# Performance work log

Measured on AMD Instinct MI355X. Metric: run time of the kernel, lower is better.

Reference implementation:

```python
import jax, jax.numpy as jnp
import numpy as np

H = 4096          # hidden_size
I = 14336         # intermediate_size
G = 128           # quantization group size along the input dim


def dequant(q, s, g=G):
    """Dequantize group-scaled int4 weights.
    q: [out, in] int (values in [-8, 7]); s: [out, in//g] float scales.
    Returns fp weight [out, in]: W[o, i] = q[o, i] * s[o, i // g].
    """
    O, In = q.shape
    return (q.reshape(O, In // g, g).astype(s.dtype) * s[:, :, None]).reshape(O, In)


def setup_inputs() -> dict:
    key = jax.random.key(0)
    ks = jax.random.split(key, 7)
    x = jax.random.normal(ks[0], (2, 2048, H), dtype=jnp.float32)

    def mk_qlinear(kq, ksc, out_d, in_d):
        q = jax.random.randint(kq, (out_d, in_d), -8, 8, dtype=jnp.int32)  # int4 range
        s = jax.random.uniform(ksc, (out_d, in_d // G), dtype=jnp.float32,
                               minval=0.005, maxval=0.02)
        return q, s

    gate_q, gate_s = mk_qlinear(ks[1], ks[2], I, H)
    up_q, up_s = mk_qlinear(ks[3], ks[4], I, H)
    down_q, down_s = mk_qlinear(ks[5], ks[6], H, I)
    return {"x": x,
            "gate_q": gate_q, "gate_s": gate_s,
            "up_q": up_q, "up_s": up_s,
            "down_q": down_q, "down_s": down_s}


def reference(x, gate_q, gate_s, up_q, up_s, down_q, down_s):
    # SwiGLU MLP: down( silu(gate(x)) * up(x) ) with group-dequantized weights.
    Wg = dequant(gate_q, gate_s)   # [I, H]
    Wu = dequant(up_q, up_s)       # [I, H]
    Wd = dequant(down_q, down_s)   # [H, I]
    gate_score = jax.nn.silu(jnp.einsum('bsh,ih->bsi', x, Wg))
    intermediate = gate_score * jnp.einsum('bsh,ih->bsi', x, Wu)
    return jnp.einsum('bsi,hi->bsh', intermediate, Wd)
```

## Files before the change

### kernel.cpp

```cpp
#include <hip/hip_runtime.h>
#include <hip/hip_bf16.h>


#define HDIM 4096
#define IDIM 14336
#define MTOK 4096
#define GRP 128

typedef __attribute__((ext_vector_type(8))) short bf16x8;
typedef __attribute__((ext_vector_type(4))) float f32x4;
typedef __attribute__((ext_vector_type(4))) unsigned short u16x4;

#define WAIT_LGKM0 asm volatile("s_waitcnt lgkmcnt(0)" ::: "memory")
#define WAIT_VM(N) asm volatile("s_waitcnt vmcnt(" #N ")" ::: "memory")
#define SBAR       __builtin_amdgcn_s_barrier()
#define SCHB       __builtin_amdgcn_sched_barrier(0)

__device__ __forceinline__ unsigned short f2bf(float f) {
  union { float f; unsigned int u; } v; v.f = f;
  return (unsigned short)((v.u + 0x7fffu + ((v.u >> 16) & 1u)) >> 16);
}
__device__ __forceinline__ unsigned pk2(float a, float b) {
  union { float f; unsigned u; } ua, ub; ua.f = a; ub.f = b;
  return __builtin_amdgcn_perm(ub.u, ua.u, 0x07060302u);
}

#define GLD16(G, L)                                                           \
  __builtin_amdgcn_global_load_lds(                                           \
      (const __attribute__((address_space(1))) unsigned int*)(G),             \
      (__attribute__((address_space(3))) unsigned int*)(L), 16, 0, 0)

__global__ __launch_bounds__(256) void cvt_x_kernel(const float* __restrict__ x,
                                                    unsigned short* __restrict__ xb) {
  const int n = MTOK * HDIM;
  const int stride = gridDim.x * 256 * 4;
  for (int i = (blockIdx.x * 256 + threadIdx.x) * 4; i < n; i += stride) {
    float4 v = *reinterpret_cast<const float4*>(x + i);
    u16x4 o;
    o[0] = f2bf(v.x); o[1] = f2bf(v.y); o[2] = f2bf(v.z); o[3] = f2bf(v.w);
    *reinterpret_cast<u16x4*>(xb + i) = o;
  }
}

__global__ __launch_bounds__(256) void deq_kernel(const int* __restrict__ q,
                                                  const float* __restrict__ s,
                                                  unsigned short* __restrict__ w,
                                                  int In) {
  const int row  = blockIdx.y;
  const int col0 = blockIdx.x * 2048 + threadIdx.x * 8;
  const long base = (long)row * In + col0;
  const float sc = s[row * (In / GRP) + (col0 >> 7)];
  const int4* p = (const int4*)(q + base);
  int4 a0 = p[0], a1 = p[1];
  uint4 o;
  o.x = pk2((float)a0.x * sc, (float)a0.y * sc);
  o.y = pk2((float)a0.z * sc, (float)a0.w * sc);
  o.z = pk2((float)a1.x * sc, (float)a1.y * sc);
  o.w = pk2((float)a1.z * sc, (float)a1.w * sc);
  *(uint4*)(w + base) = o;
}

__global__ __launch_bounds__(512, 2) void gateup_bf16(
    const unsigned short* __restrict__ xb,
    const unsigned short* __restrict__ wg,
    const unsigned short* __restrict__ wu,
    unsigned short* __restrict__ inter,
    const int* __restrict__ dnq, const float* __restrict__ dns,
    unsigned short* __restrict__ wdb, int nDeq)
{
  __shared__ unsigned short As[2 * 256 * 64];
  __shared__ unsigned short Bgs[2 * 128 * 64];
  __shared__ unsigned short Bus[2 * 128 * 64];

  if ((int)blockIdx.x < nDeq) {
    const long total = (long)HDIM * (IDIM / 8);
    const long stride = (long)nDeq * 512;
    for (long idx = (long)blockIdx.x * 512 + threadIdx.x; idx < total; idx += stride) {
      const long e = idx * 8;
      const int row = (int)(e / IDIM);
      const int col = (int)(e - (long)row * IDIM);
      const float sc = dns[row * (IDIM / GRP) + (col >> 7)];
      const int4* q4 = (const int4*)(dnq + (long)row * IDIM + col);
      int4 a0 = q4[0], a1 = q4[1];
      uint4 o;
      o.x = pk2((float)a0.x * sc, (float)a0.y * sc);
      o.y = pk2((float)a0.z * sc, (float)a0.w * sc);
      o.z = pk2((float)a1.x * sc, (float)a1.y * sc);
      o.w = pk2((float)a1.z * sc, (float)a1.w * sc);
      *(uint4*)(wdb + (long)row * IDIM + col) = o;
    }
    return;
  }

  const int tid = threadIdx.x, lane = tid & 63, wid = tid >> 6;
  const int wm = wid >> 1, wn = wid & 1;
  const int p = (int)blockIdx.x - nDeq;
  const int l = (p & 7) * 224 + (p >> 3);
  const int m0 = (l & 15) * 256, n0 = (l >> 4) * 128;
  const int lr = lane & 15, lc = lane >> 4;

  const int ra   = tid >> 3;
  const int scol = ((tid & 7) ^ (ra & 7)) << 3;
  const unsigned short* pa  = xb + (long)(m0 + ra) * HDIM + scol;
  const unsigned short* pbg = wg + (long)(n0 + ra) * HDIM + scol;
  const unsigned short* pbu = wu + (long)(n0 + ra) * HDIM + scol;

#define A1(KT, BUF, IT)                                                       \
  GLD16(pa + (long)(IT) * 64 * HDIM + (long)(KT) * 64,                        \
        (unsigned short*)As + (BUF) * 16384 + (IT) * 4096 + wid * 512)
#define BG1(KT, BUF, IT)                                                      \
  GLD16(pbg + (long)(IT) * 64 * HDIM + (long)(KT) * 64,                       \
        (unsigned short*)Bgs + (BUF) * 8192 + (IT) * 4096 + wid * 512)
#define BU1(KT, BUF, IT)                                                      \
  GLD16(pbu + (long)(IT) * 64 * HDIM + (long)(KT) * 64,                       \
        (unsigned short*)Bus + (BUF) * 8192 + (IT) * 4096 + wid * 512)

  f32x4 accg[4][4], accu[4][4];
  const f32x4 zero = {0.f, 0.f, 0.f, 0.f};
#pragma unroll
  for (int i = 0; i < 4; ++i)
#pragma unroll
    for (int j = 0; j < 4; ++j) { accg[i][j] = zero; accu[i][j] = zero; }

  BG1(0, 0, 0); BG1(0, 0, 1); BU1(0, 0, 0); BU1(0, 0, 1);
  A1(0, 0, 0); A1(0, 0, 1); A1(0, 0, 2); A1(0, 0, 3);
  SCHB;
  WAIT_VM(0);
  SBAR;
  SCHB;

  const int NK = HDIM / 64;
#pragma unroll 1
  for (int kt = 0; kt < NK; ++kt) {
    const int RD = kt & 1, WR = RD ^ 1;
    const int ktn = (kt + 1 < NK) ? kt + 1 : NK - 1;
    const unsigned short* Ab  = (const unsigned short*)As  + RD * 16384;
    const unsigned short* Bgb = (const unsigned short*)Bgs + RD * 8192;
    const unsigned short* Bub = (const unsigned short*)Bus + RD * 8192;
    const int soff0 = (lc ^ (lr & 7)) << 3;
    const int soff1 = ((4 + lc) ^ (lr & 7)) << 3;
    bf16x8 af[4], bg[4], bu[4];

#pragma unroll
    for (int mi = 0; mi < 4; ++mi)
      af[mi] = *(const bf16x8*)&Ab[(wm * 64 + mi * 16 + lr) * 64 + soff0];
#pragma unroll
    for (int ni = 0; ni < 4; ++ni) {
      bg[ni] = *(const bf16x8*)&Bgb[(wn * 64 + ni * 16 + lr) * 64 + soff0];
      bu[ni] = *(const bf16x8*)&Bub[(wn * 64 + ni * 16 + lr) * 64 + soff0];
    }
    BG1(ktn, WR, 0); BG1(ktn, WR, 1); BU1(ktn, WR, 0); BU1(ktn, WR, 1);
    SCHB; WAIT_LGKM0; SCHB;
    __builtin_amdgcn_s_setprio(1);
#pragma unroll
    for (int ni = 0; ni < 4; ++ni)
#pragma unroll
      for (int mi = 0; mi < 4; ++mi) {
        accg[mi][ni] = __builtin_amdgcn_mfma_f32_16x16x32_bf16(af[mi], bg[ni], accg[mi][ni], 0, 0, 0);
        accu[mi][ni] = __builtin_amdgcn_mfma_f32_16x16x32_bf16(af[mi], bu[ni], accu[mi][ni], 0, 0, 0);
      }
    __builtin_amdgcn_s_setprio(0);

#pragma unroll
    for (int mi = 0; mi < 4; ++mi)
      af[mi] = *(const bf16x8*)&Ab[(wm * 64 + mi * 16 + lr) * 64 + soff1];
#pragma unroll
    for (int ni = 0; ni < 4; ++ni) {
      bg[ni] = *(const bf16x8*)&Bgb[(wn * 64 + ni * 16 + lr) * 64 + soff1];
      bu[ni] = *(const bf16x8*)&Bub[(wn * 64 + ni * 16 + lr) * 64 + soff1];
    }
    A1(ktn, WR, 0); A1(ktn, WR, 1); A1(ktn, WR, 2); A1(ktn, WR, 3);
    SCHB; WAIT_LGKM0; SCHB;
    __builtin_amdgcn_s_setprio(1);
#pragma unroll
    for (int ni = 0; ni < 4; ++ni)
#pragma unroll
      for (int mi = 0; mi < 4; ++mi) {
        accg[mi][ni] = __builtin_amdgcn_mfma_f32_16x16x32_bf16(af[mi], bg[ni], accg[mi][ni], 0, 0, 0);
        accu[mi][ni] = __builtin_amdgcn_mfma_f32_16x16x32_bf16(af[mi], bu[ni], accu[mi][ni], 0, 0, 0);
      }
    __builtin_amdgcn_s_setprio(0);

    SCHB;
    WAIT_VM(0);
    SBAR;
    SCHB;
  }

  const int r0 = m0 + wm * 64, c0 = n0 + wn * 64;
#pragma unroll
  for (int mi = 0; mi < 4; ++mi)
#pragma unroll
    for (int ni = 0; ni < 4; ++ni)
#pragma unroll
      for (int r = 0; r < 4; ++r) {
        float g = accg[mi][ni][r], u = accu[mi][ni][r];
        float sv = g / (1.f + __expf(-g));
        int row = r0 + mi * 16 + lc * 4 + r;
        int col = c0 + ni * 16 + lr;
        inter[(long)row * IDIM + col] = f2bf(sv * u);
      }
#undef A1
#undef BG1
#undef BU1
}

__global__ __launch_bounds__(512, 2) void down_bf16(
    const unsigned short* __restrict__ inter,
    const unsigned short* __restrict__ wd,
    float* __restrict__ out)
{
  __shared__ unsigned short As[2 * 256 * 64];
  __shared__ unsigned short Bs[2 * 256 * 64];

  const int tid = threadIdx.x, lane = tid & 63, wid = tid >> 6;
  const int wm = wid >> 2, wn = wid & 3;
  const int p = blockIdx.x;
  const int l = (p & 7) * 32 + (p >> 3);
  const int m0 = (l & 15) * 256, n0 = (l >> 4) * 256;
  const int lr = lane & 15, lc = lane >> 4;

  const int ra   = tid >> 3;
  const int scol = ((tid & 7) ^ (ra & 7)) << 3;
  const unsigned short* pa = inter + (long)(m0 + ra) * IDIM + scol;
  const unsigned short* pb = wd + (long)(n0 + ra) * IDIM + scol;

#define DA1(KT, BUF, IT)                                                      \
  GLD16(pa + (long)(IT) * 64 * IDIM + (long)(KT) * 64,                        \
        (unsigned short*)As + (BUF) * 16384 + (IT) * 4096 + wid * 512)
#define DB1(KT, BUF, IT)                                                      \
  GLD16(pb + (long)(IT) * 64 * IDIM + (long)(KT) * 64,                        \
        (unsigned short*)Bs + (BUF) * 16384 + (IT) * 4096 + wid * 512)

  f32x4 acc[8][4];
  const f32x4 zero = {0.f, 0.f, 0.f, 0.f};
#pragma unroll
  for (int i = 0; i < 8; ++i)
#pragma unroll
    for (int j = 0; j < 4; ++j) acc[i][j] = zero;

  DB1(0, 0, 0); DB1(0, 0, 1); DB1(0, 0, 2); DB1(0, 0, 3);
  DA1(0, 0, 0); DA1(0, 0, 1); DA1(0, 0, 2); DA1(0, 0, 3);
  SCHB;
  WAIT_VM(0);
  SBAR;
  SCHB;

  const int NK = IDIM / 64;
#pragma unroll 1
  for (int kt = 0; kt < NK; ++kt) {
    const int RD = kt & 1, WR = RD ^ 1;
    const int ktn = (kt + 1 < NK) ? kt + 1 : NK - 1;
    const unsigned short* Ab = (const unsigned short*)As + RD * 16384;
    const unsigned short* Bb = (const unsigned short*)Bs + RD * 16384;
    const int soff0 = (lc ^ (lr & 7)) << 3;
    const int soff1 = ((4 + lc) ^ (lr & 7)) << 3;
    bf16x8 af[8], bfr[4];

#pragma unroll
    for (int mi = 0; mi < 8; ++mi)
      af[mi] = *(const bf16x8*)&Ab[(wm * 128 + mi * 16 + lr) * 64 + soff0];
#pragma unroll
    for (int ni = 0; ni < 4; ++ni)
      bfr[ni] = *(const bf16x8*)&Bb[(wn * 64 + ni * 16 + lr) * 64 + soff0];
    DB1(ktn, WR, 0); DB1(ktn, WR, 1); DB1(ktn, WR, 2); DB1(ktn, WR, 3);
    SCHB; WAIT_LGKM0; SCHB;
    __builtin_amdgcn_s_setprio(1);
#pragma unroll
    for (int ni = 0; ni < 4; ++ni)
#pragma unroll
      for (int mi = 0; mi < 8; ++mi)
        acc[mi][ni] = __builtin_amdgcn_mfma_f32_16x16x32_bf16(af[mi], bfr[ni], acc[mi][ni], 0, 0, 0);
    __builtin_amdgcn_s_setprio(0);

#pragma unroll
    for (int mi = 0; mi < 8; ++mi)
      af[mi] = *(const bf16x8*)&Ab[(wm * 128 + mi * 16 + lr) * 64 + soff1];
#pragma unroll
    for (int ni = 0; ni < 4; ++ni)
      bfr[ni] = *(const bf16x8*)&Bb[(wn * 64 + ni * 16 + lr) * 64 + soff1];
    DA1(ktn, WR, 0); DA1(ktn, WR, 1); DA1(ktn, WR, 2); DA1(ktn, WR, 3);
    SCHB; WAIT_LGKM0; SCHB;
    __builtin_amdgcn_s_setprio(1);
#pragma unroll
    for (int ni = 0; ni < 4; ++ni)
#pragma unroll
      for (int mi = 0; mi < 8; ++mi)
        acc[mi][ni] = __builtin_amdgcn_mfma_f32_16x16x32_bf16(af[mi], bfr[ni], acc[mi][ni], 0, 0, 0);
    __builtin_amdgcn_s_setprio(0);

    SCHB;
    WAIT_VM(0);
    SBAR;
    SCHB;
  }

  const int r0 = m0 + wm * 128, c0 = n0 + wn * 64;
#pragma unroll
  for (int mi = 0; mi < 8; ++mi)
#pragma unroll
    for (int ni = 0; ni < 4; ++ni)
#pragma unroll
      for (int r = 0; r < 4; ++r) {
        int row = r0 + mi * 16 + lc * 4 + r;
        int col = c0 + ni * 16 + lr;
        out[(long)row * HDIM + col] = acc[mi][ni][r];
      }
#undef DA1
#undef DB1
}

extern "C" void kernel_launch(void* const* d_in, const int* in_sizes, int n_in,
                              void* d_out, int out_size, void* d_ws, size_t ws_size,
                              hipStream_t stream) {
  const float* x   = (const float*)d_in[0];
  const int*   gq  = (const int*)d_in[1];
  const float* gsc = (const float*)d_in[2];
  const int*   uq  = (const int*)d_in[3];
  const float* usc = (const float*)d_in[4];
  const int*   dq  = (const int*)d_in[5];
  const float* dsc = (const float*)d_in[6];
  float* out = (float*)d_out;

  unsigned short* xb    = (unsigned short*)d_ws;
  unsigned short* inter = xb + (size_t)MTOK * HDIM;
  unsigned short* wgb   = inter + (size_t)MTOK * IDIM;
  unsigned short* wub   = wgb + (size_t)IDIM * HDIM;
  unsigned short* wdb   = wub + (size_t)IDIM * HDIM;
  const size_t needOverlap = ((size_t)MTOK * HDIM + (size_t)MTOK * IDIM +
                              3 * (size_t)IDIM * HDIM) * 2;

  hipLaunchKernelGGL(cvt_x_kernel, dim3(2048), dim3(256), 0, stream, x, xb);
  hipLaunchKernelGGL(deq_kernel, dim3(HDIM / 2048, IDIM), dim3(256), 0, stream,
                     gq, gsc, wgb, HDIM);
  hipLaunchKernelGGL(deq_kernel, dim3(HDIM / 2048, IDIM), dim3(256), 0, stream,
                     uq, usc, wub, HDIM);

  if (ws_size >= needOverlap) {
    hipLaunchKernelGGL(gateup_bf16, dim3(256 + 1792), dim3(512), 0, stream,
                       xb, wgb, wub, inter, dq, dsc, wdb, 256);
    hipLaunchKernelGGL(down_bf16, dim3(256), dim3(512), 0, stream,
                       inter, wdb, out);
  } else {
    hipLaunchKernelGGL(gateup_bf16, dim3(1792), dim3(512), 0, stream,
                       xb, wgb, wub, inter, dq, dsc, wgb, 0);
    hipLaunchKernelGGL(deq_kernel, dim3(IDIM / 2048, HDIM), dim3(256), 0, stream,
                       dq, dsc, wgb, IDIM);
    hipLaunchKernelGGL(down_bf16, dim3(256), dim3(512), 0, stream,
                       inter, wgb, out);
  }
}
```

Measured before the change: 1.374 ms.

## Split fused gate/up GEMM into separate 256x256-tile GEMMs with deferred SwiGLU epilogue

Replaces the fused gate+up kernel, which used 256x128 tiles with dual accumulators, with two separate GEMMs. Both use the larger 256x256 tile shape taken from the down GEMM, through a shared macro body. The gate GEMM writes bf16 pre-activations into the intermediate buffer. The up GEMM reads them back, applies SiLU and the product, and writes the result in its epilogue. The up-weight dequantization moves into spare blocks of the gate kernel alongside the down-weight dequant, so it overlaps with gate compute instead of running as its own launch. In exchange, the intermediate buffer makes an extra round-trip through memory, there is one more launch, and the gate values are rounded to bf16 before SiLU, which changes precision slightly.

```diff
diff --git a/kernel.cpp b/kernel.cpp
--- a/kernel.cpp
+++ b/kernel.cpp
@@ -19,6 +19,10 @@
 __device__ __forceinline__ unsigned short f2bf(float f) {
   union { float f; unsigned int u; } v; v.f = f;
   return (unsigned short)((v.u + 0x7fffu + ((v.u >> 16) & 1u)) >> 16);
+}
+__device__ __forceinline__ float bf2f(unsigned short b) {
+  union { unsigned int u; float f; } v; v.u = ((unsigned int)b) << 16;
+  return v.f;
 }
 __device__ __forceinline__ unsigned pk2(float a, float b) {
   union { float f; unsigned u; } ua, ub; ua.f = a; ub.f = b;
@@ -60,254 +64,170 @@
   *(uint4*)(w + base) = o;
 }
 
-__global__ __launch_bounds__(512, 2) void gateup_bf16(
-    const unsigned short* __restrict__ xb,
-    const unsigned short* __restrict__ wg,
-    const unsigned short* __restrict__ wu,
-    unsigned short* __restrict__ inter,
+__device__ __forceinline__ void deq_embedded(const int* __restrict__ q,
+                                             const float* __restrict__ s,
+                                             unsigned short* __restrict__ w,
+                                             int In, int bid, int nBlk) {
+  const long total = (long)IDIM * HDIM / 8;
+  const long stride = (long)nBlk * 512;
+  for (long idx = (long)bid * 512 + threadIdx.x; idx < total; idx += stride) {
+    const long e = idx * 8;
+    const int row = (int)(e / In);
+    const int col = (int)(e - (long)row * In);
+    const float sc = s[row * (In / GRP) + (col >> 7)];
+    const int4* q4 = (const int4*)(q + (long)row * In + col);
+    int4 a0 = q4[0], a1 = q4[1];
+    uint4 o;
+    o.x = pk2((float)a0.x * sc, (float)a0.y * sc);
+    o.y = pk2((float)a0.z * sc, (float)a0.w * sc);
+    o.z = pk2((float)a1.x * sc, (float)a1.y * sc);
+    o.w = pk2((float)a1.z * sc, (float)a1.w * sc);
+    *(uint4*)(w + (long)row * In + col) = o;
+  }
+}
+
+#define GEMM_BODY(LDA_, NK_, EPI_)                                            \
+  const int tid = threadIdx.x, lane = tid & 63, wid = tid >> 6;               \
+  const int wm = wid >> 2, wn = wid & 3;                                      \
+  const int lr = lane & 15, lc = lane >> 4;                                   \
+  const int ra   = tid >> 3;                                                  \
+  const int scol = ((tid & 7) ^ (ra & 7)) << 3;                               \
+  const unsigned short* pa = Abase + (long)(m0 + ra) * (LDA_) + scol;         \
+  const unsigned short* pb = Bbase + (long)(n0 + ra) * (LDA_) + scol;         \
+  f32x4 acc[8][4];                                                            \
+  const f32x4 zero = {0.f, 0.f, 0.f, 0.f};                                    \
+  _Pragma("unroll")                                                           \
+  for (int i = 0; i < 8; ++i)                                                 \
+    _Pragma("unroll")                                                         \
+    for (int j = 0; j < 4; ++j) acc[i][j] = zero;                             \
+  GB1(0, 0, 0); GB1(0, 0, 1); GB1(0, 0, 2); GB1(0, 0, 3);                     \
+  GA1(0, 0, 0); GA1(0, 0, 1); GA1(0, 0, 2); GA1(0, 0, 3);                     \
+  SCHB; WAIT_VM(0); SBAR; SCHB;                                               \
+  _Pragma("unroll 1")                                                         \
+  for (int kt = 0; kt < (NK_); ++kt) {                                        \
+    const int RD = kt & 1, WR = RD ^ 1;                                       \
+    const int ktn = (kt + 1 < (NK_)) ? kt + 1 : (NK_)-1;                      \
+    const unsigned short* Ab = (const unsigned short*)As + RD * 16384;        \
+    const unsigned short* Bb = (const unsigned short*)Bs + RD * 16384;        \
+    const int soff0 = (lc ^ (lr & 7)) << 3;                                   \
+    const int soff1 = ((4 + lc) ^ (lr & 7)) << 3;                             \
+    bf16x8 af[8], bfr[4];                                                     \
+    _Pragma("unroll")                                                         \
+    for (int mi = 0; mi < 8; ++mi)                                            \
+      af[mi] = *(const bf16x8*)&Ab[(wm * 128 + mi * 16 + lr) * 64 + soff0];   \
+    _Pragma("unroll")                                                         \
+    for (int ni = 0; ni < 4; ++ni)                                            \
+      bfr[ni] = *(const bf16x8*)&Bb[(wn * 64 + ni * 16 + lr) * 64 + soff0];   \
+    GB1(ktn, WR, 0); GB1(ktn, WR, 1); GB1(ktn, WR, 2); GB1(ktn, WR, 3);       \
+    SCHB; WAIT_LGKM0; SCHB;                                                   \
+    __builtin_amdgcn_s_setprio(1);                                            \
+    _Pragma("unroll")                                                         \
+    for (int ni = 0; ni < 4; ++ni)                                            \
+      _Pragma("unroll")                                                       \
+      for (int mi = 0; mi < 8; ++mi)                                          \
+        acc[mi][ni] = __builtin_amdgcn_mfma_f32_16x16x32_bf16(af[mi], bfr[ni], acc[mi][ni], 0, 0, 0); \
+    __builtin_amdgcn_s_setprio(0);                                            \
+    _Pragma("unroll")                                                         \
+    for (int mi = 0; mi < 8; ++mi)                                            \
+      af[mi] = *(const bf16x8*)&Ab[(wm * 128 + mi * 16 + lr) * 64 + soff1];   \
+    _Pragma("unroll")                                                         \
+    for (int ni = 0; ni < 4; ++ni)                                            \
+      bfr[ni] = *(const bf16x8*)&Bb[(wn * 64 + ni * 16 + lr) * 64 + soff1];   \
+    GA1(ktn, WR, 0); GA1(ktn, WR, 1); GA1(ktn, WR, 2); GA1(ktn, WR, 3);       \
+    SCHB; WAIT_LGKM0; SCHB;                                                   \
+    __builtin_amdgcn_s_setprio(1);                                            \
+    _Pragma("unroll")                                                         \
+    for (int ni = 0; ni < 4; ++ni)                                            \
+      _Pragma("unroll")                                                       \
+      for (int mi = 0; mi < 8; ++mi)                                          \
+        acc[mi][ni] = __builtin_amdgcn_mfma_f32_16x16x32_bf16(af[mi], bfr[ni], acc[mi][ni], 0, 0, 0); \
+    __builtin_amdgcn_s_setprio(0);                                            \
+    SCHB; WAIT_VM(0); SBAR; SCHB;                                             \
+  }                                                                           \
+  const int r0 = m0 + wm * 128, c0 = n0 + wn * 64;                            \
+  _Pragma("unroll")                                                           \
+  for (int mi = 0; mi < 8; ++mi)                                              \
+    _Pragma("unroll")                                                         \
+    for (int ni = 0; ni < 4; ++ni)                                            \
+      _Pragma("unroll")                                                       \
+      for (int r = 0; r < 4; ++r) {                                           \
+        int row = r0 + mi * 16 + lc * 4 + r;                                  \
+        int col = c0 + ni * 16 + lr;                                          \
+        if ((EPI_) == 0) {                                                    \
+          interb[(long)row * IDIM + col] = f2bf(acc[mi][ni][r]);              \
+        } else if ((EPI_) == 1) {                                             \
+          float g = bf2f(interb[(long)row * IDIM + col]);                     \
+          float sv = g / (1.f + __expf(-g));                                  \
+          interb[(long)row * IDIM + col] = f2bf(sv * acc[mi][ni][r]);         \
+        } else {                                                              \
+          outf[(long)row * HDIM + col] = acc[mi][ni][r];                      \
+        }                                                                     \
+      }
+
+#define GA1(KT, BUF, IT)                                                      \
+  GLD16(pa + (long)(IT) * 64 * lda + (long)(KT) * 64,                         \
+        (unsigned short*)As + (BUF) * 16384 + (IT) * 4096 + wid * 512)
+#define GB1(KT, BUF, IT)                                                      \
+  GLD16(pb + (long)(IT) * 64 * lda + (long)(KT) * 64,                         \
+        (unsigned short*)Bs + (BUF) * 16384 + (IT) * 4096 + wid * 512)
+
+__global__ __launch_bounds__(512, 2) void gate_gemm(
+    const unsigned short* __restrict__ Abase,
+    const unsigned short* __restrict__ Bbase,
+    unsigned short* __restrict__ interb,
+    const int* __restrict__ uq, const float* __restrict__ usc,
+    unsigned short* __restrict__ wub,
     const int* __restrict__ dnq, const float* __restrict__ dns,
     unsigned short* __restrict__ wdb, int nDeq)
 {
   __shared__ unsigned short As[2 * 256 * 64];
-  __shared__ unsigned short Bgs[2 * 128 * 64];
-  __shared__ unsigned short Bus[2 * 128 * 64];
+  __shared__ unsigned short Bs[2 * 256 * 64];
+  float* outf = nullptr; (void)outf;
+  const int lda = HDIM;
 
   if ((int)blockIdx.x < nDeq) {
-    const long total = (long)HDIM * (IDIM / 8);
-    const long stride = (long)nDeq * 512;
-    for (long idx = (long)blockIdx.x * 512 + threadIdx.x; idx < total; idx += stride) {
-      const long e = idx * 8;
-      const int row = (int)(e / IDIM);
-      const int col = (int)(e - (long)row * IDIM);
-      const float sc = dns[row * (IDIM / GRP) + (col >> 7)];
-      const int4* q4 = (const int4*)(dnq + (long)row * IDIM + col);
-      int4 a0 = q4[0], a1 = q4[1];
-      uint4 o;
-      o.x = pk2((float)a0.x * sc, (float)a0.y * sc);
-      o.y = pk2((float)a0.z * sc, (float)a0.w * sc);
-      o.z = pk2((float)a1.x * sc, (float)a1.y * sc);
-      o.w = pk2((float)a1.z * sc, (float)a1.w * sc);
-      *(uint4*)(wdb + (long)row * IDIM + col) = o;
-    }
+    const int half = nDeq >> 1;
+    if ((int)blockIdx.x < half)
+      deq_embedded(uq, usc, wub, HDIM, blockIdx.x, half);
+    else
+      deq_embedded(dnq, dns, wdb, IDIM, blockIdx.x - half, nDeq - half);
     return;
   }
-
-  const int tid = threadIdx.x, lane = tid & 63, wid = tid >> 6;
-  const int wm = wid >> 1, wn = wid & 1;
   const int p = (int)blockIdx.x - nDeq;
-  const int l = (p & 7) * 224 + (p >> 3);
-  const int m0 = (l & 15) * 256, n0 = (l >> 4) * 128;
-  const int lr = lane & 15, lc = lane >> 4;
-
-  const int ra   = tid >> 3;
-  const int scol = ((tid & 7) ^ (ra & 7)) << 3;
-  const unsigned short* pa  = xb + (long)(m0 + ra) * HDIM + scol;
-  const unsigned short* pbg = wg + (long)(n0 + ra) * HDIM + scol;
-  const unsigned short* pbu = wu + (long)(n0 + ra) * HDIM + scol;
-
-#define A1(KT, BUF, IT)                                                       \
-  GLD16(pa + (long)(IT) * 64 * HDIM + (long)(KT) * 64,                        \
-        (unsigned short*)As + (BUF) * 16384 + (IT) * 4096 + wid * 512)
-#define BG1(KT, BUF, IT)                                                      \
-  GLD16(pbg + (long)(IT) * 64 * HDIM + (long)(KT) * 64,                       \
-        (unsigned short*)Bgs + (BUF) * 8192 + (IT) * 4096 + wid * 512)
-#define BU1(KT, BUF, IT)                                                      \
-  GLD16(pbu + (long)(IT) * 64 * HDIM + (long)(KT) * 64,                       \
-        (unsigned short*)Bus + (BUF) * 8192 + (IT) * 4096 + wid * 512)
-
-  f32x4 accg[4][4], accu[4][4];
-  const f32x4 zero = {0.f, 0.f, 0.f, 0.f};
-#pragma unroll
-  for (int i = 0; i < 4; ++i)
-#pragma unroll
-    for (int j = 0; j < 4; ++j) { accg[i][j] = zero; accu[i][j] = zero; }
-
-  BG1(0, 0, 0); BG1(0, 0, 1); BU1(0, 0, 0); BU1(0, 0, 1);
-  A1(0, 0, 0); A1(0, 0, 1); A1(0, 0, 2); A1(0, 0, 3);
-  SCHB;
-  WAIT_VM(0);
-  SBAR;
-  SCHB;
-
-  const int NK = HDIM / 64;
-#pragma unroll 1
-  for (int kt = 0; kt < NK; ++kt) {
-    const int RD = kt & 1, WR = RD ^ 1;
-    const int ktn = (kt + 1 < NK) ? kt + 1 : NK - 1;
-    const unsigned short* Ab  = (const unsigned short*)As  + RD * 16384;
-    const unsigned short* Bgb = (const unsigned short*)Bgs + RD * 8192;
-    const unsigned short* Bub = (const unsigned short*)Bus + RD * 8192;
-    const int soff0 = (lc ^ (lr & 7)) << 3;
-    const int soff1 = ((4 + lc) ^ (lr & 7)) << 3;
-    bf16x8 af[4], bg[4], bu[4];
-
-#pragma unroll
-    for (int mi = 0; mi < 4; ++mi)
-      af[mi] = *(const bf16x8*)&Ab[(wm * 64 + mi * 16 + lr) * 64 + soff0];
-#pragma unroll
-    for (int ni = 0; ni < 4; ++ni) {
-      bg[ni] = *(const bf16x8*)&Bgb[(wn * 64 + ni * 16 + lr) * 64 + soff0];
-      bu[ni] = *(const bf16x8*)&Bub[(wn * 64 + ni * 16 + lr) * 64 + soff0];
-    }
-    BG1(ktn, WR, 0); BG1(ktn, WR, 1); BU1(ktn, WR, 0); BU1(ktn, WR, 1);
-    SCHB; WAIT_LGKM0; SCHB;
-    __builtin_amdgcn_s_setprio(1);
-#pragma unroll
-    for (int ni = 0; ni < 4; ++ni)
-#pragma unroll
-      for (int mi = 0; mi < 4; ++mi) {
-        accg[mi][ni] = __builtin_amdgcn_mfma_f32_16x16x32_bf16(af[mi], bg[ni], accg[mi][ni], 0, 0, 0);
-        accu[mi][ni] = __builtin_amdgcn_mfma_f32_16x16x32_bf16(af[mi], bu[ni], accu[mi][ni], 0, 0, 0);
-      }
-    __builtin_amdgcn_s_setprio(0);
-
-#pragma unroll
-    for (int mi = 0; mi < 4; ++mi)
-      af[mi] = *(const bf16x8*)&Ab[(wm * 64 + mi * 16 + lr) * 64 + soff1];
-#pragma unroll
-    for (int ni = 0; ni < 4; ++ni) {
-      bg[ni] = *(const bf16x8*)&Bgb[(wn * 64 + ni * 16 + lr) * 64 + soff1];
-      bu[ni] = *(const bf16x8*)&Bub[(wn * 64 + ni * 16 + lr) * 64 + soff1];
-    }
-    A1(ktn, WR, 0); A1(ktn, WR, 1); A1(ktn, WR, 2); A1(ktn, WR, 3);
-    SCHB; WAIT_LGKM0; SCHB;
-    __builtin_amdgcn_s_setprio(1);
-#pragma unroll
-    for (int ni = 0; ni < 4; ++ni)
-#pragma unroll
-      for (int mi = 0; mi < 4; ++mi) {
-        accg[mi][ni] = __builtin_amdgcn_mfma_f32_16x16x32_bf16(af[mi], bg[ni], accg[mi][ni], 0, 0, 0);
-        accu[mi][ni] = __builtin_amdgcn_mfma_f32_16x16x32_bf16(af[mi], bu[ni], accu[mi][ni], 0, 0, 0);
-      }
-    __builtin_amdgcn_s_setprio(0);
-
-    SCHB;
-    WAIT_VM(0);
-    SBAR;
-    SCHB;
-  }
-
-  const int r0 = m0 + wm * 64, c0 = n0 + wn * 64;
-#pragma unroll
-  for (int mi = 0; mi < 4; ++mi)
-#pragma unroll
-    for (int ni = 0; ni < 4; ++ni)
-#pragma unroll
-      for (int r = 0; r < 4; ++r) {
-        float g = accg[mi][ni][r], u = accu[mi][ni][r];
-        float sv = g / (1.f + __expf(-g));
-        int row = r0 + mi * 16 + lc * 4 + r;
-        int col = c0 + ni * 16 + lr;
-        inter[(long)row * IDIM + col] = f2bf(sv * u);
-      }
-#undef A1
-#undef BG1
-#undef BU1
-}
-
-__global__ __launch_bounds__(512, 2) void down_bf16(
-    const unsigned short* __restrict__ inter,
-    const unsigned short* __restrict__ wd,
+  const int l = (p & 7) * 112 + (p >> 3);
+  const int m0 = (l & 15) * 256, n0 = (l >> 4) * 256;
+  GEMM_BODY(HDIM, HDIM / 64, 0)
+}
+
+__global__ __launch_bounds__(512, 2) void up_gemm(
+    const unsigned short* __restrict__ Abase,
+    const unsigned short* __restrict__ Bbase,
+    unsigned short* __restrict__ interb)
+{
+  __shared__ unsigned short As[2 * 256 * 64];
+  __shared__ unsigned short Bs[2 * 256 * 64];
+  float* outf = nullptr; (void)outf;
+  const int lda = HDIM;
+  const int p = (int)blockIdx.x;
+  const int l = (p & 7) * 112 + (p >> 3);
+  const int m0 = (l & 15) * 256, n0 = (l >> 4) * 256;
+  GEMM_BODY(HDIM, HDIM / 64, 1)
+}
+
+__global__ __launch_bounds__(512, 2) void down_gemm(
+    const unsigned short* __restrict__ Abase,
+    const unsigned short* __restrict__ Bbase,
     float* __restrict__ out)
 {
   __shared__ unsigned short As[2 * 256 * 64];
   __shared__ unsigned short Bs[2 * 256 * 64];
-
-  const int tid = threadIdx.x, lane = tid & 63, wid = tid >> 6;
-  const int wm = wid >> 2, wn = wid & 3;
-  const int p = blockIdx.x;
+  unsigned short* interb = nullptr; (void)interb;
+  float* outf = out;
+  const int lda = IDIM;
+  const int p = (int)blockIdx.x;
   const int l = (p & 7) * 32 + (p >> 3);
   const int m0 = (l & 15) * 256, n0 = (l >> 4) * 256;
-  const int lr = lane & 15, lc = lane >> 4;
-
-  const int ra   = tid >> 3;
-  const int scol = ((tid & 7) ^ (ra & 7)) << 3;
-  const unsigned short* pa = inter + (long)(m0 + ra) * IDIM + scol;
-  const unsigned short* pb = wd + (long)(n0 + ra) * IDIM + scol;
-
-#define DA1(KT, BUF, IT)                                                      \
-  GLD16(pa + (long)(IT) * 64 * IDIM + (long)(KT) * 64,                        \
-        (unsigned short*)As + (BUF) * 16384 + (IT) * 4096 + wid * 512)
-#define DB1(KT, BUF, IT)                                                      \
-  GLD16(pb + (long)(IT) * 64 * IDIM + (long)(KT) * 64,                        \
-        (unsigned short*)Bs + (BUF) * 16384 + (IT) * 4096 + wid * 512)
-
-  f32x4 acc[8][4];
-  const f32x4 zero = {0.f, 0.f, 0.f, 0.f};
-#pragma unroll
-  for (int i = 0; i < 8; ++i)
-#pragma unroll
-    for (int j = 0; j < 4; ++j) acc[i][j] = zero;
-
-  DB1(0, 0, 0); DB1(0, 0, 1); DB1(0, 0, 2); DB1(0, 0, 3);
-  DA1(0, 0, 0); DA1(0, 0, 1); DA1(0, 0, 2); DA1(0, 0, 3);
-  SCHB;
-  WAIT_VM(0);
-  SBAR;
-  SCHB;
-
-  const int NK = IDIM / 64;
-#pragma unroll 1
-  for (int kt = 0; kt < NK; ++kt) {
-    const int RD = kt & 1, WR = RD ^ 1;
-    const int ktn = (kt + 1 < NK) ? kt + 1 : NK - 1;
-    const unsigned short* Ab = (const unsigned short*)As + RD * 16384;
-    const unsigned short* Bb = (const unsigned short*)Bs + RD * 16384;
-    const int soff0 = (lc ^ (lr & 7)) << 3;
-    const int soff1 = ((4 + lc) ^ (lr & 7)) << 3;
-    bf16x8 af[8], bfr[4];
-
-#pragma unroll
-    for (int mi = 0; mi < 8; ++mi)
-      af[mi] = *(const bf16x8*)&Ab[(wm * 128 + mi * 16 + lr) * 64 + soff0];
-#pragma unroll
-    for (int ni = 0; ni < 4; ++ni)
-      bfr[ni] = *(const bf16x8*)&Bb[(wn * 64 + ni * 16 + lr) * 64 + soff0];
-    DB1(ktn, WR, 0); DB1(ktn, WR, 1); DB1(ktn, WR, 2); DB1(ktn, WR, 3);
-    SCHB; WAIT_LGKM0; SCHB;
-    __builtin_amdgcn_s_setprio(1);
-#pragma unroll
-    for (int ni = 0; ni < 4; ++ni)
-#pragma unroll
-      for (int mi = 0; mi < 8; ++mi)
-        acc[mi][ni] = __builtin_amdgcn_mfma_f32_16x16x32_bf16(af[mi], bfr[ni], acc[mi][ni], 0, 0, 0);
-    __builtin_amdgcn_s_setprio(0);
-
-#pragma unroll
-    for (int mi = 0; mi < 8; ++mi)
-      af[mi] = *(const bf16x8*)&Ab[(wm * 128 + mi * 16 + lr) * 64 + soff1];
-#pragma unroll
-    for (int ni = 0; ni < 4; ++ni)
-      bfr[ni] = *(const bf16x8*)&Bb[(wn * 64 + ni * 16 + lr) * 64 + soff1];
-    DA1(ktn, WR, 0); DA1(ktn, WR, 1); DA1(ktn, WR, 2); DA1(ktn, WR, 3);
-    SCHB; WAIT_LGKM0; SCHB;
-    __builtin_amdgcn_s_setprio(1);
-#pragma unroll
-    for (int ni = 0; ni < 4; ++ni)
-#pragma unroll
-      for (int mi = 0; mi < 8; ++mi)
-        acc[mi][ni] = __builtin_amdgcn_mfma_f32_16x16x32_bf16(af[mi], bfr[ni], acc[mi][ni], 0, 0, 0);
-    __builtin_amdgcn_s_setprio(0);
-
-    SCHB;
-    WAIT_VM(0);
-    SBAR;
-    SCHB;
-  }
-
-  const int r0 = m0 + wm * 128, c0 = n0 + wn * 64;
-#pragma unroll
-  for (int mi = 0; mi < 8; ++mi)
-#pragma unroll
-    for (int ni = 0; ni < 4; ++ni)
-#pragma unroll
-      for (int r = 0; r < 4; ++r) {
-        int row = r0 + mi * 16 + lc * 4 + r;
-        int col = c0 + ni * 16 + lr;
-        out[(long)row * HDIM + col] = acc[mi][ni][r];
-      }
-#undef DA1
-#undef DB1
+  GEMM_BODY(IDIM, IDIM / 64, 2)
 }
 
 extern "C" void kernel_launch(void* const* d_in, const int* in_sizes, int n_in,
@@ -333,20 +253,24 @@
   hipLaunchKernelGGL(cvt_x_kernel, dim3(2048), dim3(256), 0, stream, x, xb);
   hipLaunchKernelGGL(deq_kernel, dim3(HDIM / 2048, IDIM), dim3(256), 0, stream,
                      gq, gsc, wgb, HDIM);
-  hipLaunchKernelGGL(deq_kernel, dim3(HDIM / 2048, IDIM), dim3(256), 0, stream,
-                     uq, usc, wub, HDIM);
 
   if (ws_size >= needOverlap) {
-    hipLaunchKernelGGL(gateup_bf16, dim3(256 + 1792), dim3(512), 0, stream,
-                       xb, wgb, wub, inter, dq, dsc, wdb, 256);
-    hipLaunchKernelGGL(down_bf16, dim3(256), dim3(512), 0, stream,
+    hipLaunchKernelGGL(gate_gemm, dim3(512 + 896), dim3(512), 0, stream,
+                       xb, wgb, inter, uq, usc, wub, dq, dsc, wdb, 512);
+    hipLaunchKernelGGL(up_gemm, dim3(896), dim3(512), 0, stream,
+                       xb, wub, inter);
+    hipLaunchKernelGGL(down_gemm, dim3(256), dim3(512), 0, stream,
                        inter, wdb, out);
   } else {
-    hipLaunchKernelGGL(gateup_bf16, dim3(1792), dim3(512), 0, stream,
-                       xb, wgb, wub, inter, dq, dsc, wgb, 0);
+    hipLaunchKernelGGL(deq_kernel, dim3(HDIM / 2048, IDIM), dim3(256), 0, stream,
+                       uq, usc, wub, HDIM);
+    hipLaunchKernelGGL(gate_gemm, dim3(896), dim3(512), 0, stream,
+                       xb, wgb, inter, uq, usc, wub, dq, dsc, wub, 0);
+    hipLaunchKernelGGL(up_gemm, dim3(896), dim3(512), 0, stream,
+                       xb, wub, inter);
     hipLaunchKernelGGL(deq_kernel, dim3(IDIM / 2048, HDIM), dim3(256), 0, stream,
                        dq, dsc, wgb, IDIM);
-    hipLaunchKernelGGL(down_bf16, dim3(256), dim3(512), 0, stream,
+    hipLaunchKernelGGL(down_gemm, dim3(256), dim3(512), 0, stream,
                        inter, wgb, out);
   }
 }
```

Measured after the change: 1.492 ms. +8.6%, slower.
